# Kernel optimization log

Measured on AMD Instinct MI355X. Metric: run time of the kernel, lower is better.

## Reference

```python
import jax, jax.numpy as jnp
import numpy as np

N, D_IN, H, M = 16384, 360, 512, 2048


def _linear(x, W, b):
    return x @ W.T + b


def _bidir_softmax(Q, K):
    # score[i, j] = <Q_i, K_j>
    s = Q @ K.T                      # [N, M]
    return jax.nn.softmax(s, axis=0), jax.nn.softmax(s, axis=1)


def _read(Q, K):
    sq, sm = _bidir_softmax(Q, K)
    upd = Q * (jax.lax.stop_gradient(sm) @ K)   # elementwise gate by attended memory
    return upd, sq, sm


def _un_read(Q, K):
    # scores computed against -K, but memory combine still uses K (as in torch source)
    sq, sm = _bidir_softmax(Q, -K)
    upd = Q * (jax.lax.stop_gradient(sm) @ K)
    return upd, sq, sm


def _upload(Q, K):
    sq, sm = _bidir_softmax(Q, K)
    m, d = K.shape
    g = jnp.argmax(sm, axis=1)                       # top-1 slot per query  [N]
    col_max = jnp.max(sq, axis=0)                    # max over queries per slot [m]
    n = Q.shape[0]
    w = sq[jnp.arange(n), g] / col_max[g]            # per-query weight [N]
    # vectorized form of the per-slot python loop: scatter-reduce weighted queries
    query_update = jax.ops.segment_sum(w[:, None] * Q, g, num_segments=m)  # [m, d]
    upd = query_update + K
    norm = jnp.linalg.norm(upd, axis=1, keepdims=True)
    upd = upd / jnp.maximum(norm, 1e-12)             # F.normalize(dim=1)
    return jax.lax.stop_gradient(upd)


def setup_inputs() -> dict:
    key = jax.random.key(0)
    ks = jax.random.split(key, 12)
    s = 0.02
    return {
        "x": jax.random.normal(ks[0], (N, D_IN), jnp.float32),
        "m_items_1": jax.random.normal(ks[1], (M, H), jnp.float32),
        "W1": jax.random.normal(ks[2], (H, D_IN), jnp.float32) * s,
        "b1": jnp.zeros((H,), jnp.float32),
        "W2": jax.random.normal(ks[3], (H, H), jnp.float32) * s,
        "b2": jnp.zeros((H,), jnp.float32),
        "W3": jax.random.normal(ks[4], (H, H), jnp.float32) * s,
        "b3": jnp.zeros((H,), jnp.float32),
        "Wd": jax.random.normal(ks[5], (1, H), jnp.float32) * s,
        "bd": jnp.zeros((1,), jnp.float32),
        "train": 1,
    }


def reference(x, m_items_1, W1, b1, W2, b2, W3, b3, Wd, bd, train):
    h = jax.nn.relu(_linear(x, W1, b1))
    h = jax.nn.relu(_linear(h, W2, b2))   # dropout=0.0 -> identity
    h = jax.nn.relu(_linear(h, W3, b3))
    pred_min_p, _, _ = _read(h, m_items_1)
    pred_min_n, _, _ = _un_read(h, m_items_1)
    mem = _upload(h, m_items_1) if train else m_items_1
    pred = _linear(h, Wd, bd)
    return (pred, pred_min_n, pred_min_p, mem)
```

## Files before the change

### kernel.cpp

```cpp
#include <hip/hip_runtime.h>
#include <math.h>

#define N_ROWS 16384
#define D_INN  360
#define KP1    384
#define HID    512
#define M_SLOTS 2048

typedef __attribute__((ext_vector_type(8))) short short8v;
typedef __attribute__((ext_vector_type(4))) float f32x4;
typedef __attribute__((address_space(1))) unsigned int as1_uint;
typedef __attribute__((address_space(3))) unsigned int as3_uint;

__device__ __forceinline__ unsigned short bf16_rne(float f){
  unsigned u = __float_as_uint(f);
  unsigned r = u + 0x7FFFu + ((u >> 16) & 1u);
  return (unsigned short)(r >> 16);
}
__device__ __forceinline__ float bf16_to_f32(unsigned short h){
  return __uint_as_float(((unsigned)h) << 16);
}

__device__ __forceinline__ void glds16(const void* g, void* l){
  __builtin_amdgcn_global_load_lds((const as1_uint*)g, (as3_uint*)l, 16, 0, 0);
}

__device__ __forceinline__ float4 ld4bf(const unsigned short* hi, const unsigned short* lo, size_t off){
  uint2 h = *(const uint2*)(hi + off);
  uint2 l = *(const uint2*)(lo + off);
  float4 r;
  r.x = bf16_to_f32((unsigned short)(h.x & 0xffffu)) + bf16_to_f32((unsigned short)(l.x & 0xffffu));
  r.y = bf16_to_f32((unsigned short)(h.x >> 16))     + bf16_to_f32((unsigned short)(l.x >> 16));
  r.z = bf16_to_f32((unsigned short)(h.y & 0xffffu)) + bf16_to_f32((unsigned short)(l.y & 0xffffu));
  r.w = bf16_to_f32((unsigned short)(h.y >> 16))     + bf16_to_f32((unsigned short)(l.y >> 16));
  return r;
}


__device__ __forceinline__ void split_body(const float* __restrict__ src,
                                           unsigned short* __restrict__ hi,
                                           unsigned short* __restrict__ lo, int b){
  int idx = (b*256 + (int)threadIdx.x) * 8;
  float4 a = *(const float4*)&src[idx];
  float4 bb = *(const float4*)&src[idx+4];
  float v[8] = {a.x,a.y,a.z,a.w,bb.x,bb.y,bb.z,bb.w};
  short8v hv, lv;
#pragma unroll
  for (int e=0;e<8;++e){
    unsigned short h = bf16_rne(v[e]);
    hv[e] = (short)h;
    lv[e] = (short)bf16_rne(v[e] - bf16_to_f32(h));
  }
  *(short8v*)&hi[idx] = hv;
  *(short8v*)&lo[idx] = lv;
}

__device__ __forceinline__ void pad_split_body(const float* __restrict__ src,
                                               unsigned short* __restrict__ hi,
                                               unsigned short* __restrict__ lo,
                                               int R, int Ksrc, int Kp, int b){
  long long e0 = ((long long)b*256 + threadIdx.x) * 4;
  if (e0 >= (long long)R*Kp) return;
  int row = (int)(e0 / Kp), c = (int)(e0 % Kp);
  unsigned short h4[4], l4[4];
  if (c < Ksrc){
    float4 v = *(const float4*)&src[(size_t)row*Ksrc + c];
    float vv[4] = {v.x, v.y, v.z, v.w};
#pragma unroll
    for (int e=0;e<4;++e){
      unsigned short h = bf16_rne(vv[e]);
      h4[e] = h;
      l4[e] = bf16_rne(vv[e] - bf16_to_f32(h));
    }
  } else {
#pragma unroll
    for (int e=0;e<4;++e){ h4[e]=0; l4[e]=0; }
  }
  *(uint2*)&hi[(size_t)row*Kp + c] = *(uint2*)h4;
  *(uint2*)&lo[(size_t)row*Kp + c] = *(uint2*)l4;
}

__global__ __launch_bounds__(256) void init_all(
    const float* __restrict__ x,  const float* __restrict__ W1,
    const float* __restrict__ W2, const float* __restrict__ W3,
    const float* __restrict__ Km,
    unsigned short* __restrict__ xph,  unsigned short* __restrict__ xpl,
    unsigned short* __restrict__ W1ph, unsigned short* __restrict__ W1pl,
    unsigned short* __restrict__ W2h,  unsigned short* __restrict__ W2l,
    unsigned short* __restrict__ W3h,  unsigned short* __restrict__ W3l,
    unsigned short* __restrict__ Khi,  unsigned short* __restrict__ Klo,
    unsigned short* __restrict__ Kt,
    float* __restrict__ qacc, int* __restrict__ cnt)
{
  __shared__ float tile[64][65];
  int b = blockIdx.x;
  const int t = threadIdx.x;
  if (b < 6144){ pad_split_body(x, xph, xpl, N_ROWS, D_INN, KP1, b); return; }
  b -= 6144;
  if (b < 192){ pad_split_body(W1, W1ph, W1pl, HID, D_INN, KP1, b); return; }
  b -= 192;
  if (b < 128){ split_body(W2, W2h, W2l, b); return; }
  b -= 128;
  if (b < 128){ split_body(W3, W3h, W3l, b); return; }
  b -= 128;
  if (b < 512){ split_body(Km, Khi, Klo, b); return; }
  b -= 512;
  if (b < 256){
    const int sb = (b & 31) * 64;
    const int hb = (b >> 5) * 64;
    {
      int r = t >> 2, cq = t & 3;
#pragma unroll
      for (int q=0;q<4;++q){
        float4 v = *(const float4*)&Km[(size_t)(sb+r)*HID + hb + cq*16 + q*4];
        tile[r][cq*16+q*4+0]=v.x; tile[r][cq*16+q*4+1]=v.y;
        tile[r][cq*16+q*4+2]=v.z; tile[r][cq*16+q*4+3]=v.w;
      }
    }
    __syncthreads();
    {
      int hl = t >> 2, sq = t & 3;
      unsigned short w16[16];
#pragma unroll
      for (int q=0;q<16;++q) w16[q] = bf16_rne(tile[sq*16+q][hl]);
      *(uint4*)&Kt[(size_t)(hb+hl)*M_SLOTS + sb + sq*16]     = *(uint4*)&w16[0];
      *(uint4*)&Kt[(size_t)(hb+hl)*M_SLOTS + sb + sq*16 + 8] = *(uint4*)&w16[8];
    }
    return;
  }
  b -= 256;
  if (b < 512){
    int idx = (b*256 + t)*8;
    float4 z = {0.f,0.f,0.f,0.f};
    *(float4*)&qacc[idx]     = z;
    *(float4*)&qacc[idx + 4] = z;
    return;
  }
  b -= 512;
  { int i = b*256 + t; if (i < M_SLOTS) cnt[i] = 0; }
}

__global__ __launch_bounds__(512) void mlp_gemm(
    const unsigned short* __restrict__ Ah_g, const unsigned short* __restrict__ Al_g,
    const unsigned short* __restrict__ Wh_g, const unsigned short* __restrict__ Wl_g,
    const float* __restrict__ bias,
    unsigned short* __restrict__ Ohi, unsigned short* __restrict__ Olo,
    int Kp)
{
  __shared__ char smem[65536];
  unsigned short* Ah = (unsigned short*)smem;
  unsigned short* Al = (unsigned short*)(smem + 16384);
  unsigned short* Bh = (unsigned short*)(smem + 32768);
  unsigned short* Bl = (unsigned short*)(smem + 49152);
  const int t = threadIdx.x;
  const int lane = t & 63, w = t >> 6;
  const int l15 = lane & 15, l4 = lane >> 4;
  const int rowBase = blockIdx.x * 128;
  const int colBase = blockIdx.y * 128;
  const int wr = (w >> 1) * 32;
  const int wc = (w & 1) * 64;

  f32x4 acc[2][4];
#pragma unroll
  for (int i=0;i<2;++i)
#pragma unroll
    for (int j=0;j<4;++j) acc[i][j] = (f32x4){0.f,0.f,0.f,0.f};

  const int nkt = Kp >> 6;
  for (int kt = 0; kt < nkt; ++kt){
    const int k0 = kt * 64;
#pragma unroll
    for (int p = 0; p < 2; ++p){
      int idx = p*512 + t;
      int r = idx >> 3, c = idx & 7;
      int cc = c ^ (r & 7);
      size_t go = (size_t)(rowBase + r) * Kp + (k0 + cc*8);
      glds16(Ah_g + go, (char*)Ah + idx*16);
      glds16(Al_g + go, (char*)Al + idx*16);
    }
#pragma unroll
    for (int p = 0; p < 2; ++p){
      int idx = p*512 + t;
      int r = idx >> 3, c = idx & 7;
      int cc = c ^ (r & 7);
      size_t go = (size_t)(colBase + r) * Kp + (k0 + cc*8);
      glds16(Wh_g + go, (char*)Bh + idx*16);
      glds16(Wl_g + go, (char*)Bl + idx*16);
    }
    __syncthreads();

#pragma unroll
    for (int s = 0; s < 2; ++s){
      short8v a_h[2], a_l[2], b_h[4], b_l[4];
#pragma unroll
      for (int rt = 0; rt < 2; ++rt){
        int r = wr + rt*16 + l15;
        int off = r*128 + ((s*4 + l4) ^ (r & 7))*16;
        a_h[rt] = *(const short8v*)((const char*)Ah + off);
        a_l[rt] = *(const short8v*)((const char*)Al + off);
      }
#pragma unroll
      for (int ct = 0; ct < 4; ++ct){
        int r = wc + ct*16 + l15;
        int off = r*128 + ((s*4 + l4) ^ (r & 7))*16;
        b_h[ct] = *(const short8v*)((const char*)Bh + off);
        b_l[ct] = *(const short8v*)((const char*)Bl + off);
      }
#pragma unroll
      for (int rt = 0; rt < 2; ++rt)
#pragma unroll
        for (int ct = 0; ct < 4; ++ct){
          acc[rt][ct] = __builtin_amdgcn_mfma_f32_16x16x32_bf16(a_h[rt], b_h[ct], acc[rt][ct], 0,0,0);
          acc[rt][ct] = __builtin_amdgcn_mfma_f32_16x16x32_bf16(a_h[rt], b_l[ct], acc[rt][ct], 0,0,0);
          acc[rt][ct] = __builtin_amdgcn_mfma_f32_16x16x32_bf16(a_l[rt], b_h[ct], acc[rt][ct], 0,0,0);
        }
    }
    __syncthreads();
  }

  float bcol[4];
#pragma unroll
  for (int ct=0; ct<4; ++ct) bcol[ct] = bias[colBase + wc + ct*16 + l15];
  unsigned short* Sout = (unsigned short*)smem;
#pragma unroll
  for (int rt=0; rt<2; ++rt)
#pragma unroll
    for (int ct=0; ct<4; ++ct)
#pragma unroll
      for (int reg=0; reg<4; ++reg){
        float v = acc[rt][ct][reg] + bcol[ct];
        v = v > 0.f ? v : 0.f;
        acc[rt][ct][reg] = v;
        Sout[(wr + rt*16 + l4*4 + reg)*136 + wc + ct*16 + l15] = bf16_rne(v);
      }
  __syncthreads();
#pragma unroll
  for (int p = 0; p < 4; ++p){
    int row = (t >> 4) + p*32;
    int c8 = (t & 15) * 8;
    uint4 v = *(uint4*)&Sout[row*136 + c8];
    *(uint4*)&Ohi[(size_t)(rowBase+row)*HID + colBase + c8] = v;
  }
  __syncthreads();
#pragma unroll
  for (int rt=0; rt<2; ++rt)
#pragma unroll
    for (int ct=0; ct<4; ++ct)
#pragma unroll
      for (int reg=0; reg<4; ++reg){
        float v = acc[rt][ct][reg];
        unsigned short h = bf16_rne(v);
        Sout[(wr + rt*16 + l4*4 + reg)*136 + wc + ct*16 + l15] = bf16_rne(v - bf16_to_f32(h));
      }
  __syncthreads();
#pragma unroll
  for (int p = 0; p < 4; ++p){
    int row = (t >> 4) + p*32;
    int c8 = (t & 15) * 8;
    uint4 v = *(uint4*)&Sout[row*136 + c8];
    *(uint4*)&Olo[(size_t)(rowBase+row)*HID + colBase + c8] = v;
  }
}

__global__ __launch_bounds__(512) void sgemm_stats(
    const unsigned short* __restrict__ Qhi, const unsigned short* __restrict__ Qlo,
    const unsigned short* __restrict__ Khi, const unsigned short* __restrict__ Klo,
    unsigned short* __restrict__ Sb,
    float* __restrict__ pmax, int* __restrict__ pcol,
    float* __restrict__ psum, float* __restrict__ pnmax, float* __restrict__ pnsum,
    float* __restrict__ pcolmax)
{
  __shared__ char smem[65536];
  unsigned short* Ah = (unsigned short*)smem;
  unsigned short* Al = (unsigned short*)(smem + 16384);
  unsigned short* Bh = (unsigned short*)(smem + 32768);
  unsigned short* Bl = (unsigned short*)(smem + 49152);
  const int t = threadIdx.x;
  const int lane = t & 63, w = t >> 6;
  const int l15 = lane & 15, l4 = lane >> 4;
  const int cb = blockIdx.x;
  const int rb = blockIdx.y;
  const int rowBase = rb * 128;
  const int colBase = cb * 128;
  const int wr = (w >> 1) * 32;
  const int wc = (w & 1) * 64;

  f32x4 acc[2][4];
#pragma unroll
  for (int i=0;i<2;++i)
#pragma unroll
    for (int j=0;j<4;++j) acc[i][j] = (f32x4){0.f,0.f,0.f,0.f};

  for (int kt = 0; kt < 8; ++kt){
    const int k0 = kt * 64;
#pragma unroll
    for (int p = 0; p < 2; ++p){
      int idx = p*512 + t;
      int r = idx >> 3, c = idx & 7;
      int cc = c ^ (r & 7);
      size_t go = (size_t)(rowBase + r) * HID + (k0 + cc*8);
      glds16(Qhi + go, (char*)Ah + idx*16);
      glds16(Qlo + go, (char*)Al + idx*16);
    }
#pragma unroll
    for (int p = 0; p < 2; ++p){
      int idx = p*512 + t;
      int r = idx >> 3, c = idx & 7;
      int cc = c ^ (r & 7);
      size_t go = (size_t)(colBase + r) * HID + (k0 + cc*8);
      glds16(Khi + go, (char*)Bh + idx*16);
      glds16(Klo + go, (char*)Bl + idx*16);
    }
    __syncthreads();

#pragma unroll
    for (int s = 0; s < 2; ++s){
      short8v a_h[2], a_l[2], b_h[4], b_l[4];
#pragma unroll
      for (int rt = 0; rt < 2; ++rt){
        int r = wr + rt*16 + l15;
        int off = r*128 + ((s*4 + l4) ^ (r & 7))*16;
        a_h[rt] = *(const short8v*)((const char*)Ah + off);
        a_l[rt] = *(const short8v*)((const char*)Al + off);
      }
#pragma unroll
      for (int ct = 0; ct < 4; ++ct){
        int r = wc + ct*16 + l15;
        int off = r*128 + ((s*4 + l4) ^ (r & 7))*16;
        b_h[ct] = *(const short8v*)((const char*)Bh + off);
        b_l[ct] = *(const short8v*)((const char*)Bl + off);
      }
#pragma unroll
      for (int rt = 0; rt < 2; ++rt)
#pragma unroll
        for (int ct = 0; ct < 4; ++ct){
          acc[rt][ct] = __builtin_amdgcn_mfma_f32_16x16x32_bf16(a_h[rt], b_h[ct], acc[rt][ct], 0,0,0);
          acc[rt][ct] = __builtin_amdgcn_mfma_f32_16x16x32_bf16(a_h[rt], b_l[ct], acc[rt][ct], 0,0,0);
          acc[rt][ct] = __builtin_amdgcn_mfma_f32_16x16x32_bf16(a_l[rt], b_h[ct], acc[rt][ct], 0,0,0);
        }
    }
    __syncthreads();
  }

#pragma unroll
  for (int rt = 0; rt < 2; ++rt){
#pragma unroll
    for (int reg = 0; reg < 4; ++reg){
      float v0 = acc[rt][0][reg], v1 = acc[rt][1][reg];
      float v2 = acc[rt][2][reg], v3 = acc[rt][3][reg];
      float bvv = v0; int bcc = colBase + wc + l15;
      if (v1 > bvv){ bvv = v1; bcc = colBase + wc + 16 + l15; }
      if (v2 > bvv){ bvv = v2; bcc = colBase + wc + 32 + l15; }
      if (v3 > bvv){ bvv = v3; bcc = colBase + wc + 48 + l15; }
      float mnv = fminf(fminf(v0,v1), fminf(v2,v3));
#pragma unroll
      for (int d = 1; d < 16; d <<= 1){
        float ov = __shfl_xor(bvv, d);
        int   oc = __shfl_xor(bcc, d);
        float om = __shfl_xor(mnv, d);
        if (ov > bvv || (ov == bvv && oc < bcc)){ bvv = ov; bcc = oc; }
        mnv = fminf(mnv, om);
      }
      float sp = __expf(v0-bvv)+__expf(v1-bvv)+__expf(v2-bvv)+__expf(v3-bvv);
      float sn = __expf(mnv-v0)+__expf(mnv-v1)+__expf(mnv-v2)+__expf(mnv-v3);
#pragma unroll
      for (int d = 1; d < 16; d <<= 1){ sp += __shfl_xor(sp,d); sn += __shfl_xor(sn,d); }
      if (l15 == 0){
        int row = rowBase + wr + rt*16 + l4*4 + reg;
        size_t pi = (size_t)row*32 + cb*2 + (w & 1);
        pmax[pi] = bvv; pcol[pi] = bcc; psum[pi] = sp;
        pnmax[pi] = -mnv; pnsum[pi] = sn;
      }
    }
  }

#pragma unroll
  for (int ct = 0; ct < 4; ++ct){
    float cm = -1e30f;
#pragma unroll
    for (int rt=0; rt<2; ++rt)
#pragma unroll
      for (int reg=0; reg<4; ++reg) cm = fmaxf(cm, acc[rt][ct][reg]);
    cm = fmaxf(cm, __shfl_xor(cm, 16));
    cm = fmaxf(cm, __shfl_xor(cm, 32));
    if (l4 == 0)
      pcolmax[(size_t)(rb*4 + (w>>1))*M_SLOTS + colBase + wc + ct*16 + l15] = cm;
  }

  __syncthreads();
  unsigned short* Sout = (unsigned short*)smem;
#pragma unroll
  for (int rt=0; rt<2; ++rt)
#pragma unroll
    for (int ct=0; ct<4; ++ct)
#pragma unroll
      for (int reg=0; reg<4; ++reg)
        Sout[(wr + rt*16 + l4*4 + reg)*136 + wc + ct*16 + l15] = bf16_rne(acc[rt][ct][reg]);
  __syncthreads();
#pragma unroll
  for (int p = 0; p < 4; ++p){
    int row = (t >> 4) + p*32;
    int c8 = (t & 15) * 8;
    uint4 v = *(uint4*)&Sout[row*136 + c8];
    *(uint4*)&Sb[(size_t)(rowBase+row)*M_SLOTS + colBase + c8] = v;
  }
}

__global__ __launch_bounds__(256) void merge_all(
    const float* __restrict__ pmax, const int* __restrict__ pcol,
    const float* __restrict__ psum, const float* __restrict__ pnmax,
    const float* __restrict__ pnsum, const float* __restrict__ pcolmax,
    float* __restrict__ rowm, float* __restrict__ rsp,
    float* __restrict__ rmn, float* __restrict__ rsn, int* __restrict__ gidx,
    int* __restrict__ cnt, float* __restrict__ colmax)
{
  if (blockIdx.x < 64){
    int row = blockIdx.x*256 + threadIdx.x;
    const size_t base = (size_t)row*32;
    float m = -1e30f; int g = 0;
    for (int i=0;i<32;++i){
      float v = pmax[base+i];
      if (v > m){ m = v; g = pcol[base+i]; }
    }
    float s = 0.f;
    for (int i=0;i<32;++i) s += psum[base+i] * __expf(pmax[base+i]-m);
    float mn = -1e30f;
    for (int i=0;i<32;++i) mn = fmaxf(mn, pnmax[base+i]);
    float sn = 0.f;
    for (int i=0;i<32;++i) sn += pnsum[base+i] * __expf(pnmax[base+i]-mn);
    rowm[row]=m; gidx[row]=g; rsp[row]=1.f/s; rmn[row]=mn; rsn[row]=1.f/sn;
    atomicAdd(&cnt[g], 1);
  } else {
    int c = (blockIdx.x - 64)*256 + threadIdx.x;
    float m = -1e30f;
    for (int r=0;r<512;++r) m = fmaxf(m, pcolmax[(size_t)r*M_SLOTS + c]);
    colmax[c] = m;
  }
}

#define PV_RB 64
#define PV_HB 256
__global__ __launch_bounds__(512) void pv2(
    const unsigned short* __restrict__ Sb, const unsigned short* __restrict__ Kt,
    const float* __restrict__ rowm, const float* __restrict__ rsp,
    const float* __restrict__ rmn, const float* __restrict__ rsn,
    const unsigned short* __restrict__ Qhi, const unsigned short* __restrict__ Qlo,
    float* __restrict__ outP, float* __restrict__ outN)
{
  __shared__ char smem[49152];
  unsigned short* Ktile = (unsigned short*)smem;
  unsigned short* Wp = (unsigned short*)(smem + 32768);
  unsigned short* Wn = (unsigned short*)(smem + 40960);
  const int t = threadIdx.x, lane = t & 63, w = t >> 6;
  const int l15 = lane & 15, l4 = lane >> 4;
  const int rowBase = blockIdx.y * PV_RB;
  const int hBase = blockIdx.x * PV_HB;
  const int wrq = (w >> 2) * 32;
  const int hw = (w & 3) * 64;
  const int rS = t >> 3;
  const int c8 = t & 7;
  const float mp = rowm[rowBase + rS], mn = rmn[rowBase + rS];

  f32x4 accP[2][4], accN[2][4];
#pragma unroll
  for (int i=0;i<2;++i)
#pragma unroll
    for (int j=0;j<4;++j){ accP[i][j]=(f32x4){0.f,0.f,0.f,0.f}; accN[i][j]=(f32x4){0.f,0.f,0.f,0.f}; }

  for (int kt = 0; kt < 32; ++kt){
    const int k0 = kt*64;
#pragma unroll
    for (int p=0;p<4;++p){
      int idx = p*512 + t;
      int r = idx >> 3, c = idx & 7;
      int cc = c ^ (r & 7);
      glds16(Kt + (size_t)(hBase + r)*M_SLOTS + k0 + cc*8, (char*)Ktile + idx*16);
    }
    short8v sv = *(const short8v*)&Sb[(size_t)(rowBase + rS)*M_SLOTS + k0 + c8*8];
    short8v wp, wn;
#pragma unroll
    for (int e=0;e<8;++e){
      float sval = bf16_to_f32((unsigned short)sv[e]);
      wp[e] = (short)bf16_rne(__expf(sval - mp));
      wn[e] = (short)bf16_rne(__expf(-sval - mn));
    }
    {
      int ch = rS*8 + (c8 ^ (rS & 7));
      *(short8v*)(Wp + ch*8) = wp;
      *(short8v*)(Wn + ch*8) = wn;
    }
    __syncthreads();
#pragma unroll
    for (int s=0; s<2; ++s){
      short8v ap[2], an[2], b[4];
#pragma unroll
      for (int rt=0; rt<2; ++rt){
        int r = wrq + rt*16 + l15;
        int ch = r*8 + ((s*4 + l4) ^ (r & 7));
        ap[rt] = *(const short8v*)(Wp + ch*8);
        an[rt] = *(const short8v*)(Wn + ch*8);
      }
#pragma unroll
      for (int ct=0; ct<4; ++ct){
        int hr = hw + ct*16 + l15;
        b[ct] = *(const short8v*)((const char*)Ktile + hr*128 + ((s*4 + l4) ^ (hr & 7))*16);
      }
#pragma unroll
      for (int rt=0; rt<2; ++rt)
#pragma unroll
        for (int ct=0; ct<4; ++ct){
          accP[rt][ct] = __builtin_amdgcn_mfma_f32_16x16x32_bf16(ap[rt], b[ct], accP[rt][ct], 0,0,0);
          accN[rt][ct] = __builtin_amdgcn_mfma_f32_16x16x32_bf16(an[rt], b[ct], accN[rt][ct], 0,0,0);
        }
    }
    __syncthreads();
  }

  float isp[2][4], isn[2][4];
#pragma unroll
  for (int rt=0; rt<2; ++rt)
#pragma unroll
    for (int reg=0; reg<4; ++reg){
      int row = rowBase + wrq + rt*16 + l4*4 + reg;
      isp[rt][reg] = rsp[row];
      isn[rt][reg] = rsn[row];
    }
  float* Pout = (float*)smem;
#pragma unroll
  for (int sign=0; sign<2; ++sign){
#pragma unroll
    for (int rh=0; rh<2; ++rh){
      if ((w >> 2) == rh){
#pragma unroll
        for (int rt=0; rt<2; ++rt)
#pragma unroll
          for (int ct=0; ct<4; ++ct)
#pragma unroll
            for (int reg=0; reg<4; ++reg){
              float v = sign ? accN[rt][ct][reg]*isn[rt][reg]
                             : accP[rt][ct][reg]*isp[rt][reg];
              Pout[(rt*16 + l4*4 + reg)*260 + hw + ct*16 + l15] = v;
            }
      }
      __syncthreads();
      float* outX = sign ? outN : outP;
#pragma unroll
      for (int p=0; p<4; ++p){
        int row = t >> 4;
        int col = (t & 15)*4 + p*64;
        int grow = rowBase + rh*32 + row;
        float4 pv = *(float4*)&Pout[row*260 + col];
        float4 qv = ld4bf(Qhi, Qlo, (size_t)grow*HID + hBase + col);
        float4 o; o.x=pv.x*qv.x; o.y=pv.y*qv.y; o.z=pv.z*qv.z; o.w=pv.w*qv.w;
        *(float4*)&outX[(size_t)grow*HID + hBase + col] = o;
      }
      __syncthreads();
    }
  }
}


__global__ __launch_bounds__(256) void csr_scan(const int* __restrict__ cnt,
                                                int* __restrict__ off, int* __restrict__ woff){
  __shared__ int partial[256];
  const int t = threadIdx.x;
  const int base = t*8;
  int local[8]; int s = 0;
#pragma unroll
  for (int j=0;j<8;++j){ local[j] = s; s += cnt[base+j]; }
  partial[t] = s;
  __syncthreads();
  for (int d=1; d<256; d<<=1){
    int v = (t>=d) ? partial[t-d] : 0;
    __syncthreads();
    partial[t] += v;
    __syncthreads();
  }
  int pre = (t==0) ? 0 : partial[t-1];
#pragma unroll
  for (int j=0;j<8;++j){ int o = pre + local[j]; off[base+j]=o; woff[base+j]=o; }
  if (t==255) off[2048] = partial[255];
}

__global__ __launch_bounds__(256) void csr_fill(const int* __restrict__ gidx,
                                                const float* __restrict__ rowm,
                                                const float* __restrict__ colmax,
                                                int* __restrict__ woff,
                                                int* __restrict__ rows, float* __restrict__ wv,
                                                int* __restrict__ sid){
  int i = blockIdx.x*256 + threadIdx.x;
  int g = gidx[i];
  int p = atomicAdd(&woff[g], 1);
  rows[p] = i;
  wv[p] = __expf(rowm[i] - colmax[g]);
  sid[p] = g;
}

__global__ __launch_bounds__(256) void upload_scatter(
    const unsigned short* __restrict__ Qhi, const unsigned short* __restrict__ Qlo,
    const int* __restrict__ sid, const int* __restrict__ rows, const float* __restrict__ wv,
    const int* __restrict__ train, float* __restrict__ qacc)
{
  if (*train == 0) return;
  const int b = blockIdx.x, t = threadIdx.x;
  __shared__ int   s_sid[64];
  __shared__ int   s_row[64];
  __shared__ float s_w[64];
  if (t < 64){
    int p = b*64 + t;
    s_sid[t] = sid[p];
    s_row[t] = rows[p];
    s_w[t]   = wv[p];
  }
  __syncthreads();
  const int h0 = t*2;
  float a0 = 0.f, a1 = 0.f;
  int prev = s_sid[0];
#pragma unroll 4
  for (int p = 0; p < 64; ++p){
    int s = s_sid[p];
    if (s != prev){
      atomicAdd(&qacc[(size_t)prev*HID + h0],     a0);
      atomicAdd(&qacc[(size_t)prev*HID + h0 + 1], a1);
      a0 = 0.f; a1 = 0.f; prev = s;
    }
    int row = s_row[p];
    float w = s_w[p];
    unsigned h = *(const unsigned*)(Qhi + (size_t)row*HID + h0);
    unsigned l = *(const unsigned*)(Qlo + (size_t)row*HID + h0);
    a0 += w * (bf16_to_f32((unsigned short)(h & 0xffffu)) + bf16_to_f32((unsigned short)(l & 0xffffu)));
    a1 += w * (bf16_to_f32((unsigned short)(h >> 16))     + bf16_to_f32((unsigned short)(l >> 16)));
  }
  atomicAdd(&qacc[(size_t)prev*HID + h0],     a0);
  atomicAdd(&qacc[(size_t)prev*HID + h0 + 1], a1);
}

__global__ __launch_bounds__(256) void upload_finish(const float* __restrict__ qacc,
                                                     const float* __restrict__ Km,
                                                     const int* __restrict__ train,
                                                     float* __restrict__ mem)
{
  const int m = blockIdx.x, t = threadIdx.x;
  const int h0 = t * 2;
  float2 kv = *(const float2*)&Km[(size_t)m*HID + h0];
  if (*train == 0){
    mem[(size_t)m*HID + h0]     = kv.x;
    mem[(size_t)m*HID + h0 + 1] = kv.y;
    return;
  }
  float2 av = *(const float2*)&qacc[(size_t)m*HID + h0];
  float v0 = av.x + kv.x, v1 = av.y + kv.y;
  __shared__ float red[256];
  red[t] = v0*v0 + v1*v1;
  __syncthreads();
  for (int s = 128; s > 0; s >>= 1){
    if (t < s) red[t] += red[t + s];
    __syncthreads();
  }
  float rinv = 1.f / fmaxf(sqrtf(red[0]), 1e-12f);
  mem[(size_t)m*HID + h0]     = v0 * rinv;
  mem[(size_t)m*HID + h0 + 1] = v1 * rinv;
}

__global__ __launch_bounds__(256) void pred_kernel(const unsigned short* __restrict__ Qhi,
                                                   const unsigned short* __restrict__ Qlo,
                                                   const float* __restrict__ Wd,
                                                   const float* __restrict__ bd,
                                                   float* __restrict__ pred)
{
  const int w = threadIdx.x >> 6, lane = threadIdx.x & 63;
  const int row = blockIdx.x * 4 + w;
  size_t base = (size_t)row * HID + lane*8;
  float4 a = ld4bf(Qhi, Qlo, base);
  float4 b = ld4bf(Qhi, Qlo, base + 4);
  float4 wa = *(const float4*)&Wd[lane*8];
  float4 wb = *(const float4*)&Wd[lane*8 + 4];
  float p = a.x*wa.x + a.y*wa.y + a.z*wa.z + a.w*wa.w
          + b.x*wb.x + b.y*wb.y + b.z*wb.z + b.w*wb.w;
#pragma unroll
  for (int d = 32; d > 0; d >>= 1) p += __shfl_down(p, d);
  if (lane == 0) pred[row] = p + bd[0];
}


extern "C" void kernel_launch(void* const* d_in, const int* in_sizes, int n_in,
                              void* d_out, int out_size, void* d_ws, size_t ws_size,
                              hipStream_t stream)
{
  const float* x   = (const float*)d_in[0];
  const float* Km  = (const float*)d_in[1];
  const float* W1  = (const float*)d_in[2];
  const float* b1  = (const float*)d_in[3];
  const float* W2  = (const float*)d_in[4];
  const float* b2  = (const float*)d_in[5];
  const float* W3  = (const float*)d_in[6];
  const float* b3  = (const float*)d_in[7];
  const float* Wd  = (const float*)d_in[8];
  const float* bd  = (const float*)d_in[9];
  const int* train = (const int*)d_in[10];

  float* out  = (float*)d_out;
  float* pred = out;
  float* outN = out + 16384;
  float* outP = out + 16384 + 8388608;
  float* memo = out + 16384 + 2*8388608;

  char* ws = (char*)d_ws;
  unsigned short* Qhi   = (unsigned short*)(ws + 0);
  unsigned short* Qlo   = (unsigned short*)(ws + 16777216);
  unsigned short* xph   = (unsigned short*)(ws + 33554432);
  unsigned short* xpl   = (unsigned short*)(ws + 46137344);
  unsigned short* h1h   = (unsigned short*)(ws + 58720256);
  unsigned short* h1l   = (unsigned short*)(ws + 75497472);
  unsigned short* h2h   = (unsigned short*)(ws + 92274688);
  unsigned short* h2l   = (unsigned short*)(ws + 109051904);
  unsigned short* Sb    = (unsigned short*)(ws + 33554432);
  unsigned short* Khi   = (unsigned short*)(ws + 125829120);
  unsigned short* Klo   = (unsigned short*)(ws + 127926272);
  unsigned short* Kt    = (unsigned short*)(ws + 130023424);
  unsigned short* W1ph  = (unsigned short*)(ws + 132120576);
  unsigned short* W1pl  = (unsigned short*)(ws + 132513792);
  unsigned short* W2h   = (unsigned short*)(ws + 132907008);
  unsigned short* W2l   = (unsigned short*)(ws + 133431296);
  unsigned short* W3h   = (unsigned short*)(ws + 133955584);
  unsigned short* W3l   = (unsigned short*)(ws + 134479872);
  float* pmax    = (float*)(ws + 135004160);
  int*   pcol    = (int*)  (ws + 137101312);
  float* psum    = (float*)(ws + 139198464);
  float* pnmax   = (float*)(ws + 141295616);
  float* pnsum   = (float*)(ws + 143392768);
  float* pcolmax = (float*)(ws + 145489920);
  float* rowm    = (float*)(ws + 149684224);
  float* rsp     = (float*)(ws + 149749760);
  float* rmn     = (float*)(ws + 149815296);
  float* rsn     = (float*)(ws + 149880832);
  int*   gidx    = (int*)  (ws + 149946368);
  float* colmax  = (float*)(ws + 150011904);
  int*   cnt     = (int*)  (ws + 150020096);
  int*   off     = (int*)  (ws + 150028288);
  int*   woff    = (int*)  (ws + 150036736);
  int*   rows    = (int*)  (ws + 150044928);
  float* wv      = (float*)(ws + 150110464);
  int*   sid     = (int*)  (ws + 150176000);
  float* qacc    = (float*)(ws + 150241536);
  const size_t NEED = 154435840ull;
  if (ws_size < NEED) return;

  dim3 blk(256);

  init_all<<<7880, blk, 0, stream>>>(x, W1, W2, W3, Km,
                                     xph, xpl, W1ph, W1pl, W2h, W2l, W3h, W3l,
                                     Khi, Klo, Kt, qacc, cnt);

  mlp_gemm<<<dim3(N_ROWS/128, 4), dim3(512), 0, stream>>>(xph, xpl, W1ph, W1pl, b1, h1h, h1l, KP1);
  mlp_gemm<<<dim3(N_ROWS/128, 4), dim3(512), 0, stream>>>(h1h, h1l, W2h, W2l, b2, h2h, h2l, HID);
  mlp_gemm<<<dim3(N_ROWS/128, 4), dim3(512), 0, stream>>>(h2h, h2l, W3h, W3l, b3, Qhi, Qlo, HID);

  sgemm_stats<<<dim3(16, 128), dim3(512), 0, stream>>>(Qhi, Qlo, Khi, Klo, Sb,
                                                       pmax, pcol, psum, pnmax, pnsum, pcolmax);
  merge_all<<<72, blk, 0, stream>>>(pmax, pcol, psum, pnmax, pnsum, pcolmax,
                                    rowm, rsp, rmn, rsn, gidx, cnt, colmax);
  pv2<<<dim3(2, 256), dim3(512), 0, stream>>>(Sb, Kt, rowm, rsp, rmn, rsn, Qhi, Qlo, outP, outN);

  csr_scan<<<1, blk, 0, stream>>>(cnt, off, woff);
  csr_fill<<<N_ROWS/256, blk, 0, stream>>>(gidx, rowm, colmax, woff, rows, wv, sid);
  upload_scatter<<<N_ROWS/64, blk, 0, stream>>>(Qhi, Qlo, sid, rows, wv, train, qacc);
  upload_finish<<<M_SLOTS, blk, 0, stream>>>(qacc, Km, train, memo);

  pred_kernel<<<N_ROWS/4, blk, 0, stream>>>(Qhi, Qlo, Wd, bd, pred);
}
```

Baseline: 474.4 us.

## Fuse pred into last MLP GEMM and use atomic column max

The column-max reduction across row blocks becomes a global atomicMax on order-preserving uint-mapped floats inside the score GEMM. This removes the large partial-colmax buffer and the serial merge blocks that scanned it. The prediction dot product with Wd is computed from fp32 activations in the final MLP GEMM epilogue as per-warp partials and summed in merge_all, which eliminates the separate pred kernel and its reread of Q. The cost is atomic contention on 2048 addresses and a small extra epilogue in the GEMM.

```diff
diff --git a/kernel.cpp b/kernel.cpp
--- a/kernel.cpp
+++ b/kernel.cpp
@@ -19,6 +19,15 @@
 }
 __device__ __forceinline__ float bf16_to_f32(unsigned short h){
   return __uint_as_float(((unsigned)h) << 16);
+}
+
+__device__ __forceinline__ unsigned fmap(float f){
+  unsigned u = __float_as_uint(f);
+  return (u & 0x80000000u) ? ~u : (u | 0x80000000u);
+}
+__device__ __forceinline__ float funmap(unsigned u){
+  unsigned b = (u & 0x80000000u) ? (u ^ 0x80000000u) : ~u;
+  return __uint_as_float(b);
 }
 
 __device__ __forceinline__ void glds16(const void* g, void* l){
@@ -90,7 +99,8 @@
     unsigned short* __restrict__ W3h,  unsigned short* __restrict__ W3l,
     unsigned short* __restrict__ Khi,  unsigned short* __restrict__ Klo,
     unsigned short* __restrict__ Kt,
-    float* __restrict__ qacc, int* __restrict__ cnt)
+    float* __restrict__ qacc, int* __restrict__ cnt,
+    unsigned* __restrict__ colmaxU)
 {
   __shared__ float tile[64][65];
   int b = blockIdx.x;
@@ -137,7 +147,7 @@
     return;
   }
   b -= 512;
-  { int i = b*256 + t; if (i < M_SLOTS) cnt[i] = 0; }
+  { int i = b*256 + t; if (i < M_SLOTS){ cnt[i] = 0; colmaxU[i] = 0u; } }
 }
 
 __global__ __launch_bounds__(512) void mlp_gemm(
@@ -145,7 +155,7 @@
     const unsigned short* __restrict__ Wh_g, const unsigned short* __restrict__ Wl_g,
     const float* __restrict__ bias,
     unsigned short* __restrict__ Ohi, unsigned short* __restrict__ Olo,
-    int Kp)
+    int Kp, const float* __restrict__ Wd, float* __restrict__ ppart)
 {
   __shared__ char smem[65536];
   unsigned short* Ah = (unsigned short*)smem;
@@ -233,6 +243,26 @@
         acc[rt][ct][reg] = v;
         Sout[(wr + rt*16 + l4*4 + reg)*136 + wc + ct*16 + l15] = bf16_rne(v);
       }
+
+  if (ppart){
+    float wdv[4];
+#pragma unroll
+    for (int ct=0; ct<4; ++ct) wdv[ct] = Wd[colBase + wc + ct*16 + l15];
+#pragma unroll
+    for (int rt=0; rt<2; ++rt)
+#pragma unroll
+      for (int reg=0; reg<4; ++reg){
+        float pd = acc[rt][0][reg]*wdv[0] + acc[rt][1][reg]*wdv[1]
+                 + acc[rt][2][reg]*wdv[2] + acc[rt][3][reg]*wdv[3];
+#pragma unroll
+        for (int d=1; d<16; d<<=1) pd += __shfl_xor(pd, d);
+        if (l15 == 0){
+          int row = rowBase + wr + rt*16 + l4*4 + reg;
+          ppart[(size_t)row*8 + (colBase >> 7)*2 + (wc >> 6)] = pd;
+        }
+      }
+  }
+
   __syncthreads();
 #pragma unroll
   for (int p = 0; p < 4; ++p){
@@ -268,7 +298,7 @@
     unsigned short* __restrict__ Sb,
     float* __restrict__ pmax, int* __restrict__ pcol,
     float* __restrict__ psum, float* __restrict__ pnmax, float* __restrict__ pnsum,
-    float* __restrict__ pcolmax)
+    unsigned* __restrict__ colmaxU)
 {
   __shared__ char smem[65536];
   unsigned short* Ah = (unsigned short*)smem;
@@ -384,7 +414,7 @@
     cm = fmaxf(cm, __shfl_xor(cm, 16));
     cm = fmaxf(cm, __shfl_xor(cm, 32));
     if (l4 == 0)
-      pcolmax[(size_t)(rb*4 + (w>>1))*M_SLOTS + colBase + wc + ct*16 + l15] = cm;
+      atomicMax(&colmaxU[colBase + wc + ct*16 + l15], fmap(cm));
   }
 
   __syncthreads();
@@ -409,33 +439,32 @@
 __global__ __launch_bounds__(256) void merge_all(
     const float* __restrict__ pmax, const int* __restrict__ pcol,
     const float* __restrict__ psum, const float* __restrict__ pnmax,
-    const float* __restrict__ pnsum, const float* __restrict__ pcolmax,
+    const float* __restrict__ pnsum,
     float* __restrict__ rowm, float* __restrict__ rsp,
     float* __restrict__ rmn, float* __restrict__ rsn, int* __restrict__ gidx,
-    int* __restrict__ cnt, float* __restrict__ colmax)
+    int* __restrict__ cnt,
+    const float* __restrict__ ppart, const float* __restrict__ bd,
+    float* __restrict__ pred)
 {
-  if (blockIdx.x < 64){
-    int row = blockIdx.x*256 + threadIdx.x;
-    const size_t base = (size_t)row*32;
-    float m = -1e30f; int g = 0;
-    for (int i=0;i<32;++i){
-      float v = pmax[base+i];
-      if (v > m){ m = v; g = pcol[base+i]; }
-    }
-    float s = 0.f;
-    for (int i=0;i<32;++i) s += psum[base+i] * __expf(pmax[base+i]-m);
-    float mn = -1e30f;
-    for (int i=0;i<32;++i) mn = fmaxf(mn, pnmax[base+i]);
-    float sn = 0.f;
-    for (int i=0;i<32;++i) sn += pnsum[base+i] * __expf(pnmax[base+i]-mn);
-    rowm[row]=m; gidx[row]=g; rsp[row]=1.f/s; rmn[row]=mn; rsn[row]=1.f/sn;
-    atomicAdd(&cnt[g], 1);
-  } else {
-    int c = (blockIdx.x - 64)*256 + threadIdx.x;
-    float m = -1e30f;
-    for (int r=0;r<512;++r) m = fmaxf(m, pcolmax[(size_t)r*M_SLOTS + c]);
-    colmax[c] = m;
-  }
+  int row = blockIdx.x*256 + threadIdx.x;
+  const size_t base = (size_t)row*32;
+  float m = -1e30f; int g = 0;
+  for (int i=0;i<32;++i){
+    float v = pmax[base+i];
+    if (v > m){ m = v; g = pcol[base+i]; }
+  }
+  float s = 0.f;
+  for (int i=0;i<32;++i) s += psum[base+i] * __expf(pmax[base+i]-m);
+  float mn = -1e30f;
+  for (int i=0;i<32;++i) mn = fmaxf(mn, pnmax[base+i]);
+  float sn = 0.f;
+  for (int i=0;i<32;++i) sn += pnsum[base+i] * __expf(pnmax[base+i]-mn);
+  rowm[row]=m; gidx[row]=g; rsp[row]=1.f/s; rmn[row]=mn; rsn[row]=1.f/sn;
+  atomicAdd(&cnt[g], 1);
+  float pd = bd[0];
+#pragma unroll
+  for (int i=0;i<8;++i) pd += ppart[(size_t)row*8 + i];
+  pred[row] = pd;
 }
 
 #define PV_RB 64
@@ -584,7 +613,7 @@
 
 __global__ __launch_bounds__(256) void csr_fill(const int* __restrict__ gidx,
                                                 const float* __restrict__ rowm,
-                                                const float* __restrict__ colmax,
+                                                const unsigned* __restrict__ colmaxU,
                                                 int* __restrict__ woff,
                                                 int* __restrict__ rows, float* __restrict__ wv,
                                                 int* __restrict__ sid){
@@ -592,7 +621,7 @@
   int g = gidx[i];
   int p = atomicAdd(&woff[g], 1);
   rows[p] = i;
-  wv[p] = __expf(rowm[i] - colmax[g]);
+  wv[p] = __expf(rowm[i] - funmap(colmaxU[g]));
   sid[p] = g;
 }
 
@@ -660,26 +689,6 @@
   float rinv = 1.f / fmaxf(sqrtf(red[0]), 1e-12f);
   mem[(size_t)m*HID + h0]     = v0 * rinv;
   mem[(size_t)m*HID + h0 + 1] = v1 * rinv;
-}
-
-__global__ __launch_bounds__(256) void pred_kernel(const unsigned short* __restrict__ Qhi,
-                                                   const unsigned short* __restrict__ Qlo,
-                                                   const float* __restrict__ Wd,
-                                                   const float* __restrict__ bd,
-                                                   float* __restrict__ pred)
-{
-  const int w = threadIdx.x >> 6, lane = threadIdx.x & 63;
-  const int row = blockIdx.x * 4 + w;
-  size_t base = (size_t)row * HID + lane*8;
-  float4 a = ld4bf(Qhi, Qlo, base);
-  float4 b = ld4bf(Qhi, Qlo, base + 4);
-  float4 wa = *(const float4*)&Wd[lane*8];
-  float4 wb = *(const float4*)&Wd[lane*8 + 4];
-  float p = a.x*wa.x + a.y*wa.y + a.z*wa.z + a.w*wa.w
-          + b.x*wb.x + b.y*wb.y + b.z*wb.z + b.w*wb.w;
-#pragma unroll
-  for (int d = 32; d > 0; d >>= 1) p += __shfl_down(p, d);
-  if (lane == 0) pred[row] = p + bd[0];
 }
 
 
@@ -729,13 +738,12 @@
   float* psum    = (float*)(ws + 139198464);
   float* pnmax   = (float*)(ws + 141295616);
   float* pnsum   = (float*)(ws + 143392768);
-  float* pcolmax = (float*)(ws + 145489920);
   float* rowm    = (float*)(ws + 149684224);
   float* rsp     = (float*)(ws + 149749760);
   float* rmn     = (float*)(ws + 149815296);
   float* rsn     = (float*)(ws + 149880832);
   int*   gidx    = (int*)  (ws + 149946368);
-  float* colmax  = (float*)(ws + 150011904);
+  unsigned* colmaxU = (unsigned*)(ws + 150011904);
   int*   cnt     = (int*)  (ws + 150020096);
   int*   off     = (int*)  (ws + 150028288);
   int*   woff    = (int*)  (ws + 150036736);
@@ -743,29 +751,31 @@
   float* wv      = (float*)(ws + 150110464);
   int*   sid     = (int*)  (ws + 150176000);
   float* qacc    = (float*)(ws + 150241536);
-  const size_t NEED = 154435840ull;
+  float* ppart   = (float*)(ws + 154435840);
+  const size_t NEED = 154960128ull;
   if (ws_size < NEED) return;
 
   dim3 blk(256);
 
   init_all<<<7880, blk, 0, stream>>>(x, W1, W2, W3, Km,
                                      xph, xpl, W1ph, W1pl, W2h, W2l, W3h, W3l,
-                                     Khi, Klo, Kt, qacc, cnt);
-
-  mlp_gemm<<<dim3(N_ROWS/128, 4), dim3(512), 0, stream>>>(xph, xpl, W1ph, W1pl, b1, h1h, h1l, KP1);
-  mlp_gemm<<<dim3(N_ROWS/128, 4), dim3(512), 0, stream>>>(h1h, h1l, W2h, W2l, b2, h2h, h2l, HID);
-  mlp_gemm<<<dim3(N_ROWS/128, 4), dim3(512), 0, stream>>>(h2h, h2l, W3h, W3l, b3, Qhi, Qlo, HID);
+                                     Khi, Klo, Kt, qacc, cnt, colmaxU);
+
+  mlp_gemm<<<dim3(N_ROWS/128, 4), dim3(512), 0, stream>>>(xph, xpl, W1ph, W1pl, b1, h1h, h1l, KP1,
+                                                          (const float*)nullptr, (float*)nullptr);
+  mlp_gemm<<<dim3(N_ROWS/128, 4), dim3(512), 0, stream>>>(h1h, h1l, W2h, W2l, b2, h2h, h2l, HID,
+                                                          (const float*)nullptr, (float*)nullptr);
+  mlp_gemm<<<dim3(N_ROWS/128, 4), dim3(512), 0, stream>>>(h2h, h2l, W3h, W3l, b3, Qhi, Qlo, HID,
+                                                          Wd, ppart);
 
   sgemm_stats<<<dim3(16, 128), dim3(512), 0, stream>>>(Qhi, Qlo, Khi, Klo, Sb,
-                                                       pmax, pcol, psum, pnmax, pnsum, pcolmax);
-  merge_all<<<72, blk, 0, stream>>>(pmax, pcol, psum, pnmax, pnsum, pcolmax,
-                                    rowm, rsp, rmn, rsn, gidx, cnt, colmax);
+                                                       pmax, pcol, psum, pnmax, pnsum, colmaxU);
+  merge_all<<<64, blk, 0, stream>>>(pmax, pcol, psum, pnmax, pnsum,
+                                    rowm, rsp, rmn, rsn, gidx, cnt, ppart, bd, pred);
   pv2<<<dim3(2, 256), dim3(512), 0, stream>>>(Sb, Kt, rowm, rsp, rmn, rsn, Qhi, Qlo, outP, outN);
 
   csr_scan<<<1, blk, 0, stream>>>(cnt, off, woff);
-  csr_fill<<<N_ROWS/256, blk, 0, stream>>>(gidx, rowm, colmax, woff, rows, wv, sid);
+  csr_fill<<<N_ROWS/256, blk, 0, stream>>>(gidx, rowm, colmaxU, woff, rows, wv, sid);
   upload_scatter<<<N_ROWS/64, blk, 0, stream>>>(Qhi, Qlo, sid, rows, wv, train, qacc);
   upload_finish<<<M_SLOTS, blk, 0, stream>>>(qacc, Km, train, memo);
-
-  pred_kernel<<<N_ROWS/4, blk, 0, stream>>>(Qhi, Qlo, Wd, bd, pred);
-}
+}
```

Result: faster. 396.4 us (-16.4%).
